# Kernel tuning notes

Hardware: AMD Instinct MI355X
Metric: run time of the kernel (lower is better)

## Reference

```python
import jax, jax.numpy as jnp
import numpy as np

NUM_FEATURES = 5
HIDDEN = 64
NUM_CLASSES = 5
N_NODES = 100000
N_EDGES = 1600000


def setup_inputs() -> dict:
    key = jax.random.key(0)
    ks = jax.random.split(key, 8)
    x = jax.random.normal(ks[0], (N_NODES, 4, NUM_FEATURES), dtype=jnp.float32)
    edge_index = jax.random.randint(ks[1], (2, N_EDGES), 0, N_NODES, dtype=jnp.int64)
    batch = jnp.zeros((N_NODES,), dtype=jnp.int64)
    # GCNConv layer 1: 5 -> 64, layer 2: 64 -> 64, output Linear: 64 -> 5
    W1 = jax.random.normal(ks[2], (NUM_FEATURES, HIDDEN), dtype=jnp.float32) / np.sqrt(NUM_FEATURES)
    b1 = jnp.zeros((HIDDEN,), dtype=jnp.float32)
    W2 = jax.random.normal(ks[3], (HIDDEN, HIDDEN), dtype=jnp.float32) / np.sqrt(HIDDEN)
    b2 = jnp.zeros((HIDDEN,), dtype=jnp.float32)
    Wout = jax.random.normal(ks[4], (HIDDEN, NUM_CLASSES), dtype=jnp.float32) / np.sqrt(HIDDEN)
    bout = jnp.zeros((NUM_CLASSES,), dtype=jnp.float32)
    return {"x": x, "edge_index": edge_index, "batch": batch,
            "W1": W1, "b1": b1, "W2": W2, "b2": b2, "Wout": Wout, "bout": bout}


def reference(x, edge_index, batch, W1, b1, W2, b2, Wout, bout):
    N = x.shape[0]
    src, dst = edge_index[0], edge_index[1]
    # GCN symmetric normalization with self-loops: deg counts incoming edges + self loop
    deg = jax.ops.segment_sum(jnp.ones(src.shape, jnp.float32), dst, num_segments=N) + 1.0
    dinv_sqrt = jax.lax.rsqrt(deg)
    norm = dinv_sqrt[src] * dinv_sqrt[dst]            # [E]
    self_norm = (1.0 / deg)[:, None]                  # self-loop weight deg^-1

    def gcn_conv(h, W, b):
        h = h @ W                                     # [N, out]
        agg = jax.ops.segment_sum(h[src] * norm[:, None], dst, num_segments=N)
        return agg + h * self_norm + b

    h = jax.nn.relu(gcn_conv(x[:, -1, :], W1, b1))    # [N, HIDDEN]
    h = jax.nn.relu(gcn_conv(h, W2, b2))              # [N, HIDDEN]
    return jax.nn.softmax(h @ Wout + bout, axis=1)    # [N, 5]
```

## Files before the change

### kernel.cpp

```cpp
#include <hip/hip_runtime.h>
#include <hip/hip_fp16.h>

#define HID 64
#define NF 5
#define NC 5

#define WSH 9
#define WINN 512
#define NBMAX 256
#define SRCB 17
#define NBLK 256


__global__ __launch_bounds__(512) void k_bcount(const int* __restrict__ dst, int E, int chunk,
                                                int nb, int* __restrict__ cntmat) {
    __shared__ int cnt[NBMAX];
    int t = threadIdx.x;
    for (int i = t; i < nb; i += 512) cnt[i] = 0;
    __syncthreads();
    int c0 = blockIdx.x * chunk;
    int c1 = c0 + chunk; if (c1 > E) c1 = E;
    for (int i = c0 + t; i < c1; i += 512)
        atomicAdd(&cnt[dst[i] >> WSH], 1);
    __syncthreads();
    for (int i = t; i < nb; i += 512) cntmat[blockIdx.x * nb + i] = cnt[i];
}

__global__ __launch_bounds__(NBLK) void k_wscan(int* __restrict__ cntmat, int nb,
                                                int* __restrict__ btot) {
    __shared__ int s[NBLK];
    int b = blockIdx.x;
    int t = threadIdx.x;
    int v = cntmat[t * nb + b];
    s[t] = v;
    __syncthreads();
    for (int o = 1; o < NBLK; o <<= 1) {
        int u = (t >= o) ? s[t - o] : 0;
        __syncthreads();
        s[t] += u;
        __syncthreads();
    }
    cntmat[t * nb + b] = s[t] - v;
    if (t == NBLK - 1) btot[b] = s[t];
}

__global__ __launch_bounds__(256) void k_bscan2(const int* __restrict__ btot, int nb, int N,
                                                int* __restrict__ bbase,
                                                int* __restrict__ offsets) {
    __shared__ int s[256];
    int t = threadIdx.x;
    int v = (t < nb) ? btot[t] : 0;
    s[t] = v;
    __syncthreads();
    for (int o = 1; o < 256; o <<= 1) {
        int u = (t >= o) ? s[t - o] : 0;
        __syncthreads();
        s[t] += u;
        __syncthreads();
    }
    if (t < nb) bbase[t] = s[t] - v;
    if (t == nb - 1) { bbase[nb] = s[t]; offsets[N] = s[t]; }
}

__global__ __launch_bounds__(512) void k_bfill(const int* __restrict__ src,
                                               const int* __restrict__ dst, int E, int chunk,
                                               int nb, const int* __restrict__ bbase,
                                               const int* __restrict__ cntmat,
                                               unsigned int* __restrict__ pairbuf) {
    __shared__ int wcur[NBMAX];
    int t = threadIdx.x;
    int blk = blockIdx.x;
    for (int i = t; i < nb; i += 512)
        wcur[i] = bbase[i] + cntmat[blk * nb + i];
    __syncthreads();
    int c0 = blk * chunk;
    int c1 = c0 + chunk; if (c1 > E) c1 = E;
    for (int i = c0 + t; i < c1; i += 512) {
        int d = dst[i];
        int b = d >> WSH;
        int p = atomicAdd(&wcur[b], 1);
        pairbuf[p] = ((unsigned)(d & (WINN - 1)) << SRCB) | (unsigned)src[i];
    }
}

__global__ __launch_bounds__(WINN) void k_csr(const unsigned int* __restrict__ pairbuf,
                                              const int* __restrict__ bbase, int N,
                                              const float* __restrict__ x,
                                              int* __restrict__ offsets,
                                              int* __restrict__ csr_src,
                                              float* __restrict__ dinv,
                                              float* __restrict__ xs) {
    int b = blockIdx.x, t = threadIdx.x;
    int winStart = b << WSH;
    int rbeg = bbase[b], rend = bbase[b + 1];
    __shared__ int deg[WINN];
    __shared__ int cur[WINN];
    __shared__ int s[WINN];
    deg[t] = 0;
    __syncthreads();
    for (int p = rbeg + t; p < rend; p += WINN)
        atomicAdd(&deg[pairbuf[p] >> SRCB], 1);
    __syncthreads();
    int v = deg[t];
    s[t] = v;
    __syncthreads();
    for (int o = 1; o < WINN; o <<= 1) {
        int u = (t >= o) ? s[t - o] : 0;
        __syncthreads();
        s[t] += u;
        __syncthreads();
    }
    int node = winStart + t;
    if (node < N) {
        int base = rbeg + s[t] - v;
        offsets[node] = base;
        cur[t] = base;
        float dv = rsqrtf((float)v + 1.0f);
        dinv[node] = dv;
        const float* xr = x + (size_t)node * (4 * NF) + 3 * NF;
#pragma unroll
        for (int k = 0; k < NF; ++k) xs[(size_t)node * NF + k] = xr[k] * dv;
    }
    __syncthreads();
    for (int p = rbeg + t; p < rend; p += WINN) {
        unsigned u = pairbuf[p];
        int dl = u >> SRCB;
        int sn = u & ((1u << SRCB) - 1);
        int pos = atomicAdd(&cur[dl], 1);
        csr_src[pos] = sn;
    }
}


__global__ __launch_bounds__(256) void k_aggX(const float* __restrict__ xs,
                                              const float* __restrict__ W1,
                                              const int* __restrict__ offsets,
                                              const int* __restrict__ csr_src,
                                              const float* __restrict__ dinv,
                                              const float* __restrict__ b1,
                                              __half* __restrict__ g1, int N) {
    int wid = (blockIdx.x * blockDim.x + threadIdx.x) >> 6;
    int lane = threadIdx.x & 63;
    int g = lane >> 3;
    int f = lane & 7;
    float w0 = W1[0 * HID + lane], w1 = W1[1 * HID + lane], w2 = W1[2 * HID + lane],
          w3 = W1[3 * HID + lane], w4 = W1[4 * HID + lane];
    if (wid >= N) return;
    int e0 = offsets[wid], e1 = offsets[wid + 1];
    bool fa = (f < NF);
    float acc = 0.f;
    int ee = e0 + g;
    int s = (ee < e1) ? csr_src[ee] : -1;
    for (int e = e0; e < e1; e += 8) {
        int cs = s;
        int en = e + 8 + g;
        s = (en < e1) ? csr_src[en] : -1;
        if (cs >= 0 && fa) acc += xs[(size_t)cs * NF + f];
    }
    if (g == 0 && fa) acc += xs[(size_t)wid * NF + f];
    acc += __shfl_xor(acc, 8, 64);
    acc += __shfl_xor(acc, 16, 64);
    acc += __shfl_xor(acc, 32, 64);
    float a0 = __shfl(acc, 0, 8), a1 = __shfl(acc, 1, 8), a2 = __shfl(acc, 2, 8),
          a3 = __shfl(acc, 3, 8), a4 = __shfl(acc, 4, 8);
    float dv = dinv[wid];
    float sres = a0 * w0 + a1 * w1 + a2 * w2 + a3 * w3 + a4 * w4;
    float r = fmaxf(fmaf(dv, sres, b1[lane]), 0.f) * dv;
    g1[(size_t)wid * HID + lane] = __float2half(r);
}

__global__ __launch_bounds__(256) void k_aggG(const __half* __restrict__ g1,
                                              const int* __restrict__ offsets,
                                              const int* __restrict__ csr_src,
                                              const float* __restrict__ dinv,
                                              float* __restrict__ aggH, int N) {
    int wid = (blockIdx.x * blockDim.x + threadIdx.x) >> 6;
    if (wid >= N) return;
    int lane = threadIdx.x & 63;
    int g = lane >> 3;
    int f8 = (lane & 7) << 3;
    int e0 = offsets[wid], e1 = offsets[wid + 1];
    float acc[8];
#pragma unroll
    for (int i = 0; i < 8; ++i) acc[i] = 0.f;
    int ee = e0 + g;
    int s = (ee < e1) ? csr_src[ee] : -1;
    for (int e = e0; e < e1; e += 8) {
        int cs = s;
        int en = e + 8 + g;
        s = (en < e1) ? csr_src[en] : -1;
        if (cs >= 0) {
            float4 raw = *reinterpret_cast<const float4*>(g1 + (size_t)cs * HID + f8);
            float2 p0 = __half22float2(*reinterpret_cast<__half2*>(&raw.x));
            float2 p1 = __half22float2(*reinterpret_cast<__half2*>(&raw.y));
            float2 p2 = __half22float2(*reinterpret_cast<__half2*>(&raw.z));
            float2 p3 = __half22float2(*reinterpret_cast<__half2*>(&raw.w));
            acc[0] += p0.x; acc[1] += p0.y; acc[2] += p1.x; acc[3] += p1.y;
            acc[4] += p2.x; acc[5] += p2.y; acc[6] += p3.x; acc[7] += p3.y;
        }
    }
#pragma unroll
    for (int o = 8; o < 64; o <<= 1) {
#pragma unroll
        for (int i = 0; i < 8; ++i) acc[i] += __shfl_xor(acc[i], o, 64);
    }
    if (lane < 8) {
        float4 raw = *reinterpret_cast<const float4*>(g1 + (size_t)wid * HID + f8);
        float2 p0 = __half22float2(*reinterpret_cast<__half2*>(&raw.x));
        float2 p1 = __half22float2(*reinterpret_cast<__half2*>(&raw.y));
        float2 p2 = __half22float2(*reinterpret_cast<__half2*>(&raw.z));
        float2 p3 = __half22float2(*reinterpret_cast<__half2*>(&raw.w));
        float dv = dinv[wid];
        float4 r0, r1;
        r0.x = dv * (acc[0] + p0.x); r0.y = dv * (acc[1] + p0.y);
        r0.z = dv * (acc[2] + p1.x); r0.w = dv * (acc[3] + p1.y);
        r1.x = dv * (acc[4] + p2.x); r1.y = dv * (acc[5] + p2.y);
        r1.z = dv * (acc[6] + p3.x); r1.w = dv * (acc[7] + p3.y);
        float4* dst4 = reinterpret_cast<float4*>(aggH + (size_t)wid * HID + f8);
        dst4[0] = r0;
        dst4[1] = r1;
    }
}

__global__ __launch_bounds__(256) void k_fuse(const float* __restrict__ aggH,
                                              const float* __restrict__ W2,
                                              const float* __restrict__ b2,
                                              const float* __restrict__ Wout,
                                              const float* __restrict__ bout,
                                              float* __restrict__ out, int N) {
    __shared__ float4 sh4[64][17];
    __shared__ float4 sW4[64 * 16];
    __shared__ float  swout[64][NC];
    __shared__ float  sb2[64];
    __shared__ float  sbout[8];
    int tx = threadIdx.x;
    int nb0 = blockIdx.x * 64;

    const float4* W2_4 = reinterpret_cast<const float4*>(W2);
    for (int i = tx; i < 64 * 16; i += 256) sW4[i] = W2_4[i];
    const float4* aggH4 = reinterpret_cast<const float4*>(aggH);
    for (int i = tx; i < 64 * 16; i += 256) {
        int row = i >> 4, c4 = i & 15;
        int node = nb0 + row;
        float4 v = {0.f, 0.f, 0.f, 0.f};
        if (node < N) v = aggH4[(size_t)node * 16 + c4];
        sh4[row][c4] = v;
    }
    if (tx < 64) sb2[tx] = b2[tx];
    for (int i = tx; i < 64 * NC; i += 256) swout[i / NC][i % NC] = Wout[i];
    if (tx < NC) sbout[tx] = bout[tx];
    __syncthreads();

    int ty = tx >> 4;
    int txl = tx & 15;

    float acc[4][4];
#pragma unroll
    for (int j = 0; j < 4; ++j)
#pragma unroll
        for (int i = 0; i < 4; ++i) acc[j][i] = 0.f;

    for (int k4 = 0; k4 < 16; ++k4) {
        float4 w0 = sW4[(k4 * 4 + 0) * 16 + txl];
        float4 w1 = sW4[(k4 * 4 + 1) * 16 + txl];
        float4 w2 = sW4[(k4 * 4 + 2) * 16 + txl];
        float4 w3 = sW4[(k4 * 4 + 3) * 16 + txl];
#pragma unroll
        for (int j = 0; j < 4; ++j) {
            float4 hq = sh4[ty * 4 + j][k4];
            acc[j][0] = fmaf(hq.x, w0.x, fmaf(hq.y, w1.x, fmaf(hq.z, w2.x, fmaf(hq.w, w3.x, acc[j][0]))));
            acc[j][1] = fmaf(hq.x, w0.y, fmaf(hq.y, w1.y, fmaf(hq.z, w2.y, fmaf(hq.w, w3.y, acc[j][1]))));
            acc[j][2] = fmaf(hq.x, w0.z, fmaf(hq.y, w1.z, fmaf(hq.z, w2.z, fmaf(hq.w, w3.z, acc[j][2]))));
            acc[j][3] = fmaf(hq.x, w0.w, fmaf(hq.y, w1.w, fmaf(hq.z, w2.w, fmaf(hq.w, w3.w, acc[j][3]))));
        }
    }

    float pl[4][NC];
#pragma unroll
    for (int j = 0; j < 4; ++j)
#pragma unroll
        for (int c = 0; c < NC; ++c) pl[j][c] = 0.f;
#pragma unroll
    for (int j = 0; j < 4; ++j) {
#pragma unroll
        for (int i = 0; i < 4; ++i) {
            int f = txl * 4 + i;
            float h2 = fmaxf(acc[j][i] + sb2[f], 0.f);
#pragma unroll
            for (int c = 0; c < NC; ++c) pl[j][c] = fmaf(h2, swout[f][c], pl[j][c]);
        }
    }
#pragma unroll
    for (int o = 1; o < 16; o <<= 1) {
#pragma unroll
        for (int j = 0; j < 4; ++j)
#pragma unroll
            for (int c = 0; c < NC; ++c) pl[j][c] += __shfl_xor(pl[j][c], o, 64);
    }
    if (txl == 0) {
#pragma unroll
        for (int j = 0; j < 4; ++j) {
            int node = nb0 + ty * 4 + j;
            if (node < N) {
                float lg[NC];
#pragma unroll
                for (int c = 0; c < NC; ++c) lg[c] = pl[j][c] + sbout[c];
                float m = lg[0];
#pragma unroll
                for (int c = 1; c < NC; ++c) m = fmaxf(m, lg[c]);
                float ssum = 0.f, ex[NC];
#pragma unroll
                for (int c = 0; c < NC; ++c) { ex[c] = __expf(lg[c] - m); ssum += ex[c]; }
                float inv = 1.0f / ssum;
#pragma unroll
                for (int c = 0; c < NC; ++c) out[(size_t)node * NC + c] = ex[c] * inv;
            }
        }
    }
}


extern "C" void kernel_launch(void* const* d_in, const int* in_sizes, int n_in,
                              void* d_out, int out_size, void* d_ws, size_t ws_size,
                              hipStream_t stream) {
    const float* x   = (const float*)d_in[0];
    const int*   ei  = (const int*)d_in[1];
    const float* W1  = (const float*)d_in[3];
    const float* b1  = (const float*)d_in[4];
    const float* W2  = (const float*)d_in[5];
    const float* b2  = (const float*)d_in[6];
    const float* Wo  = (const float*)d_in[7];
    const float* bo  = (const float*)d_in[8];
    float* out = (float*)d_out;

    const int N = in_sizes[2];
    const int E = in_sizes[1] / 2;

    size_t off = 0;
    char* base = (char*)d_ws;
    auto alloc = [&](size_t bytes) -> void* {
        off = (off + 255) & ~(size_t)255;
        void* r = base + off;
        off += bytes;
        return r;
    };
    int*      cntmat  = (int*)alloc((size_t)NBLK * NBMAX * 4);
    int*      btot    = (int*)alloc((size_t)NBMAX * 4);
    int*      bbase   = (int*)alloc(((size_t)NBMAX + 1) * 4);
    unsigned* pairbuf = (unsigned*)alloc((size_t)E * 4);
    int*      offsets = (int*)alloc(((size_t)N + 1) * 4);
    int*      csr_src = (int*)alloc((size_t)E * 4);
    float*    dinv    = (float*)alloc((size_t)N * 4);
    float*    xs      = (float*)alloc((size_t)N * NF * 4);
    __half*   g1      = (__half*)alloc((size_t)N * HID * 2);
    float*    aggH    = (float*)alloc((size_t)N * HID * 4);

    const int T = 256;
    int gNF = ((N * HID) + T - 1) / T;

    const int* src = ei;
    const int* dst = ei + E;

    int nb = (N + WINN - 1) >> WSH;
    int chunk = (E + NBLK - 1) / NBLK;

    k_bcount<<<NBLK, 512, 0, stream>>>(dst, E, chunk, nb, cntmat);
    k_wscan<<<nb, NBLK, 0, stream>>>(cntmat, nb, btot);
    k_bscan2<<<1, 256, 0, stream>>>(btot, nb, N, bbase, offsets);
    k_bfill<<<NBLK, 512, 0, stream>>>(src, dst, E, chunk, nb, bbase, cntmat, pairbuf);
    k_csr<<<nb, WINN, 0, stream>>>(pairbuf, bbase, N, x, offsets, csr_src, dinv, xs);

    k_aggX<<<gNF, T, 0, stream>>>(xs, W1, offsets, csr_src, dinv, b1, g1, N);

    k_aggG<<<gNF, T, 0, stream>>>(g1, offsets, csr_src, dinv, aggH, N);

    int nbF = (N + 63) / 64;
    k_fuse<<<nbF, 256, 0, stream>>>(aggH, W2, b2, Wo, bo, out, N);
}
```

Baseline: 218.9 us.

## Pad scaled features to 8 floats and widen edge parallelism in aggregation kernels

The first-layer input features are stored padded to 8 floats per node, so k_aggX can gather each neighbor with two float4 loads and process 32 edges per wavefront iteration instead of 8. k_aggG now processes two edge slots per lane per iteration, keeping two gathers in flight to hide memory latency. The aim is fewer loop iterations and more memory-level parallelism in the gather phases. The cost is extra memory for the padded layout and longer butterfly reductions in k_aggX.

```diff
diff --git a/kernel.cpp b/kernel.cpp
--- a/kernel.cpp
+++ b/kernel.cpp
@@ -89,7 +89,7 @@
                                               int* __restrict__ offsets,
                                               int* __restrict__ csr_src,
                                               float* __restrict__ dinv,
-                                              float* __restrict__ xs) {
+                                              float* __restrict__ xs8) {
     int b = blockIdx.x, t = threadIdx.x;
     int winStart = b << WSH;
     int rbeg = bbase[b], rend = bbase[b + 1];
@@ -118,8 +118,12 @@
         float dv = rsqrtf((float)v + 1.0f);
         dinv[node] = dv;
         const float* xr = x + (size_t)node * (4 * NF) + 3 * NF;
-#pragma unroll
-        for (int k = 0; k < NF; ++k) xs[(size_t)node * NF + k] = xr[k] * dv;
+        float4 v0, v1;
+        v0.x = xr[0] * dv; v0.y = xr[1] * dv; v0.z = xr[2] * dv; v0.w = xr[3] * dv;
+        v1.x = xr[4] * dv; v1.y = 0.f; v1.z = 0.f; v1.w = 0.f;
+        float4* xp = reinterpret_cast<float4*>(xs8 + (size_t)node * 8);
+        xp[0] = v0;
+        xp[1] = v1;
     }
     __syncthreads();
     for (int p = rbeg + t; p < rend; p += WINN) {
@@ -132,7 +136,7 @@
 }
 
 
-__global__ __launch_bounds__(256) void k_aggX(const float* __restrict__ xs,
+__global__ __launch_bounds__(256) void k_aggX(const float* __restrict__ xs8,
                                               const float* __restrict__ W1,
                                               const int* __restrict__ offsets,
                                               const int* __restrict__ csr_src,
@@ -141,28 +145,38 @@
                                               __half* __restrict__ g1, int N) {
     int wid = (blockIdx.x * blockDim.x + threadIdx.x) >> 6;
     int lane = threadIdx.x & 63;
-    int g = lane >> 3;
-    int f = lane & 7;
+    int g = lane >> 1;
+    int h = lane & 1;
     float w0 = W1[0 * HID + lane], w1 = W1[1 * HID + lane], w2 = W1[2 * HID + lane],
           w3 = W1[3 * HID + lane], w4 = W1[4 * HID + lane];
     if (wid >= N) return;
     int e0 = offsets[wid], e1 = offsets[wid + 1];
-    bool fa = (f < NF);
-    float acc = 0.f;
+    float4 acc = {0.f, 0.f, 0.f, 0.f};
     int ee = e0 + g;
     int s = (ee < e1) ? csr_src[ee] : -1;
-    for (int e = e0; e < e1; e += 8) {
+    for (int e = e0; e < e1; e += 32) {
         int cs = s;
-        int en = e + 8 + g;
+        int en = e + 32 + g;
         s = (en < e1) ? csr_src[en] : -1;
-        if (cs >= 0 && fa) acc += xs[(size_t)cs * NF + f];
-    }
-    if (g == 0 && fa) acc += xs[(size_t)wid * NF + f];
-    acc += __shfl_xor(acc, 8, 64);
-    acc += __shfl_xor(acc, 16, 64);
-    acc += __shfl_xor(acc, 32, 64);
-    float a0 = __shfl(acc, 0, 8), a1 = __shfl(acc, 1, 8), a2 = __shfl(acc, 2, 8),
-          a3 = __shfl(acc, 3, 8), a4 = __shfl(acc, 4, 8);
+        bool p = (cs >= 0);
+        int csc = p ? cs : 0;
+        float4 v = *reinterpret_cast<const float4*>(xs8 + (size_t)csc * 8 + (h << 2));
+        if (p) { acc.x += v.x; acc.y += v.y; acc.z += v.z; acc.w += v.w; }
+    }
+    if (g == 0) {
+        float4 v = *reinterpret_cast<const float4*>(xs8 + (size_t)wid * 8 + (h << 2));
+        acc.x += v.x; acc.y += v.y; acc.z += v.z; acc.w += v.w;
+    }
+#pragma unroll
+    for (int o = 2; o < 64; o <<= 1) {
+        acc.x += __shfl_xor(acc.x, o, 64);
+        acc.y += __shfl_xor(acc.y, o, 64);
+        acc.z += __shfl_xor(acc.z, o, 64);
+        acc.w += __shfl_xor(acc.w, o, 64);
+    }
+    float a0 = __shfl(acc.x, 0, 2), a1 = __shfl(acc.y, 0, 2),
+          a2 = __shfl(acc.z, 0, 2), a3 = __shfl(acc.w, 0, 2),
+          a4 = __shfl(acc.x, 1, 2);
     float dv = dinv[wid];
     float sres = a0 * w0 + a1 * w1 + a2 * w2 + a3 * w3 + a4 * w4;
     float r = fmaxf(fmaf(dv, sres, b1[lane]), 0.f) * dv;
@@ -184,19 +198,32 @@
 #pragma unroll
     for (int i = 0; i < 8; ++i) acc[i] = 0.f;
     int ee = e0 + g;
-    int s = (ee < e1) ? csr_src[ee] : -1;
-    for (int e = e0; e < e1; e += 8) {
-        int cs = s;
-        int en = e + 8 + g;
-        s = (en < e1) ? csr_src[en] : -1;
-        if (cs >= 0) {
-            float4 raw = *reinterpret_cast<const float4*>(g1 + (size_t)cs * HID + f8);
-            float2 p0 = __half22float2(*reinterpret_cast<__half2*>(&raw.x));
-            float2 p1 = __half22float2(*reinterpret_cast<__half2*>(&raw.y));
-            float2 p2 = __half22float2(*reinterpret_cast<__half2*>(&raw.z));
-            float2 p3 = __half22float2(*reinterpret_cast<__half2*>(&raw.w));
-            acc[0] += p0.x; acc[1] += p0.y; acc[2] += p1.x; acc[3] += p1.y;
-            acc[4] += p2.x; acc[5] += p2.y; acc[6] += p3.x; acc[7] += p3.y;
+    int s0 = (ee < e1) ? csr_src[ee] : -1;
+    int s1 = (ee + 8 < e1) ? csr_src[ee + 8] : -1;
+    for (int e = e0; e < e1; e += 16) {
+        int cs0 = s0, cs1 = s1;
+        int en0 = e + 16 + g, en1 = e + 24 + g;
+        s0 = (en0 < e1) ? csr_src[en0] : -1;
+        s1 = (en1 < e1) ? csr_src[en1] : -1;
+        bool p0 = (cs0 >= 0), p1 = (cs1 >= 0);
+        int c0 = p0 ? cs0 : 0, c1 = p1 ? cs1 : 0;
+        float4 raw0 = *reinterpret_cast<const float4*>(g1 + (size_t)c0 * HID + f8);
+        float4 raw1 = *reinterpret_cast<const float4*>(g1 + (size_t)c1 * HID + f8);
+        if (p0) {
+            float2 q0 = __half22float2(*reinterpret_cast<__half2*>(&raw0.x));
+            float2 q1 = __half22float2(*reinterpret_cast<__half2*>(&raw0.y));
+            float2 q2 = __half22float2(*reinterpret_cast<__half2*>(&raw0.z));
+            float2 q3 = __half22float2(*reinterpret_cast<__half2*>(&raw0.w));
+            acc[0] += q0.x; acc[1] += q0.y; acc[2] += q1.x; acc[3] += q1.y;
+            acc[4] += q2.x; acc[5] += q2.y; acc[6] += q3.x; acc[7] += q3.y;
+        }
+        if (p1) {
+            float2 q0 = __half22float2(*reinterpret_cast<__half2*>(&raw1.x));
+            float2 q1 = __half22float2(*reinterpret_cast<__half2*>(&raw1.y));
+            float2 q2 = __half22float2(*reinterpret_cast<__half2*>(&raw1.z));
+            float2 q3 = __half22float2(*reinterpret_cast<__half2*>(&raw1.w));
+            acc[0] += q0.x; acc[1] += q0.y; acc[2] += q1.x; acc[3] += q1.y;
+            acc[4] += q2.x; acc[5] += q2.y; acc[6] += q3.x; acc[7] += q3.y;
         }
     }
 #pragma unroll
@@ -206,16 +233,16 @@
     }
     if (lane < 8) {
         float4 raw = *reinterpret_cast<const float4*>(g1 + (size_t)wid * HID + f8);
-        float2 p0 = __half22float2(*reinterpret_cast<__half2*>(&raw.x));
-        float2 p1 = __half22float2(*reinterpret_cast<__half2*>(&raw.y));
-        float2 p2 = __half22float2(*reinterpret_cast<__half2*>(&raw.z));
-        float2 p3 = __half22float2(*reinterpret_cast<__half2*>(&raw.w));
+        float2 q0 = __half22float2(*reinterpret_cast<__half2*>(&raw.x));
+        float2 q1 = __half22float2(*reinterpret_cast<__half2*>(&raw.y));
+        float2 q2 = __half22float2(*reinterpret_cast<__half2*>(&raw.z));
+        float2 q3 = __half22float2(*reinterpret_cast<__half2*>(&raw.w));
         float dv = dinv[wid];
         float4 r0, r1;
-        r0.x = dv * (acc[0] + p0.x); r0.y = dv * (acc[1] + p0.y);
-        r0.z = dv * (acc[2] + p1.x); r0.w = dv * (acc[3] + p1.y);
-        r1.x = dv * (acc[4] + p2.x); r1.y = dv * (acc[5] + p2.y);
-        r1.z = dv * (acc[6] + p3.x); r1.w = dv * (acc[7] + p3.y);
+        r0.x = dv * (acc[0] + q0.x); r0.y = dv * (acc[1] + q0.y);
+        r0.z = dv * (acc[2] + q1.x); r0.w = dv * (acc[3] + q1.y);
+        r1.x = dv * (acc[4] + q2.x); r1.y = dv * (acc[5] + q2.y);
+        r1.z = dv * (acc[6] + q3.x); r1.w = dv * (acc[7] + q3.y);
         float4* dst4 = reinterpret_cast<float4*>(aggH + (size_t)wid * HID + f8);
         dst4[0] = r0;
         dst4[1] = r1;
@@ -351,7 +378,7 @@
     int*      offsets = (int*)alloc(((size_t)N + 1) * 4);
     int*      csr_src = (int*)alloc((size_t)E * 4);
     float*    dinv    = (float*)alloc((size_t)N * 4);
-    float*    xs      = (float*)alloc((size_t)N * NF * 4);
+    float*    xs8     = (float*)alloc((size_t)N * 8 * 4);
     __half*   g1      = (__half*)alloc((size_t)N * HID * 2);
     float*    aggH    = (float*)alloc((size_t)N * HID * 4);
 
@@ -368,9 +395,9 @@
     k_wscan<<<nb, NBLK, 0, stream>>>(cntmat, nb, btot);
     k_bscan2<<<1, 256, 0, stream>>>(btot, nb, N, bbase, offsets);
     k_bfill<<<NBLK, 512, 0, stream>>>(src, dst, E, chunk, nb, bbase, cntmat, pairbuf);
-    k_csr<<<nb, WINN, 0, stream>>>(pairbuf, bbase, N, x, offsets, csr_src, dinv, xs);
-
-    k_aggX<<<gNF, T, 0, stream>>>(xs, W1, offsets, csr_src, dinv, b1, g1, N);
+    k_csr<<<nb, WINN, 0, stream>>>(pairbuf, bbase, N, x, offsets, csr_src, dinv, xs8);
+
+    k_aggX<<<gNF, T, 0, stream>>>(xs8, W1, offsets, csr_src, dinv, b1, g1, N);
 
     k_aggG<<<gNF, T, 0, stream>>>(g1, offsets, csr_src, dinv, aggH, N);
 
```

Result: faster. 209.5 us (-4.3%).
